# Performance work log

Measured on AMD Instinct MI355X. Metric: run time of the kernel, lower is better.

## Reference

```python
import jax, jax.numpy as jnp
import numpy as np

H = 8       # heads
D = 512     # hidden_size
DH = D // H # head dim
FF = 2048   # hardcoded FFN hidden in source


def _layernorm(x, g, b, eps=1e-5):
    mu = jnp.mean(x, axis=-1, keepdims=True)
    var = jnp.var(x, axis=-1, keepdims=True)
    return (x - mu) * jax.lax.rsqrt(var + eps) * g + b


def setup_inputs() -> dict:
    key = jax.random.key(0)
    ks = jax.random.split(key, 12)
    B, S = 2, 4096
    s = lambda fan_in: 1.0 / np.sqrt(fan_in)
    return {
        "reaction": jax.random.normal(ks[0], (B, S, D), dtype=jnp.float32),
        "mask": jnp.ones((B, 1, 1, S), dtype=jnp.int32),
        # attention weights stored as [in, out] (torch Linear weight.T)
        "Wq": jax.random.uniform(ks[1], (D, D), jnp.float32, -s(D), s(D)),
        "Wk": jax.random.uniform(ks[2], (D, D), jnp.float32, -s(D), s(D)),
        "Wv": jax.random.uniform(ks[3], (D, D), jnp.float32, -s(D), s(D)),
        "Wo": jax.random.uniform(ks[4], (D, D), jnp.float32, -s(D), s(D)),
        "bo": jnp.zeros((D,), jnp.float32),
        "W1": jax.random.uniform(ks[5], (D, FF), jnp.float32, -s(D), s(D)),
        "b1": jnp.zeros((FF,), jnp.float32),
        "W2": jax.random.uniform(ks[6], (FF, D), jnp.float32, -s(FF), s(FF)),
        "b2": jnp.zeros((D,), jnp.float32),
        "g_sa": jnp.ones((D,), jnp.float32),
        "b_sa": jnp.zeros((D,), jnp.float32),
        "g_ff": jnp.ones((D,), jnp.float32),
        "b_ff": jnp.zeros((D,), jnp.float32),
    }


def reference(reaction, mask, Wq, Wk, Wv, Wo, bo, W1, b1, W2, b2, g_sa, b_sa, g_ff, b_ff):
    B, S, _ = reaction.shape
    # --- self-attention part (pre-norm) ---
    x = _layernorm(reaction, g_sa, b_sa)
    q = (x @ Wq).reshape(B, S, H, DH)
    k = (x @ Wk).reshape(B, S, H, DH)
    v = (x @ Wv).reshape(B, S, H, DH)
    scale = DH ** (-0.5)
    scores = jnp.einsum('bqhd,bkhd->bhqk', q * scale, k)  # [B,H,S,S]
    scores = jnp.where(mask == 0, -jnp.inf, scores)
    att = jax.nn.softmax(scores, axis=-1)
    ctx = jnp.einsum('bhqk,bkhd->bqhd', att, v).reshape(B, S, D)
    attn_out = jax.nn.gelu(ctx @ Wo + bo, approximate=False)  # GELU after output proj (as in source)
    x = attn_out + reaction
    # --- feed-forward part (pre-norm) ---
    y = _layernorm(x, g_ff, b_ff)
    y = jax.nn.gelu(y @ W1 + b1, approximate=False) @ W2 + b2
    return y + x
```

## Files before the change

### kernel.cpp

```cpp
#include <hip/hip_runtime.h>
#include <hip/hip_bf16.h>
#include <math.h>

#define HN 8
#define DM 512
#define DHD 64
#define FFD 2048
#define BB 2
#define SS 4096
#define MT (BB*SS)

typedef __bf16 bf16_t;
typedef __bf16 bf16x8 __attribute__((ext_vector_type(8)));
typedef __bf16 bf16x4 __attribute__((ext_vector_type(4)));
typedef float  floatx4 __attribute__((ext_vector_type(4)));

__device__ __forceinline__ void async_copy16(const bf16_t* g, bf16_t* l) {
  __builtin_amdgcn_global_load_lds((const __attribute__((address_space(1))) void*)g,
                                   (__attribute__((address_space(3))) void*)l,
                                   16, 0, 0);
}

#if __has_builtin(__builtin_amdgcn_exp2f)
__device__ __forceinline__ float fast_exp2(float x) { return __builtin_amdgcn_exp2f(x); }
#else
__device__ __forceinline__ float fast_exp2(float x) { return __expf(x * 0.69314718056f); }
#endif

__device__ __forceinline__ float gelu_f(float x) {
  float y = 0.7978845608f * (x + 0.044715f * x * x * x);
  float e = fast_exp2(y * 2.885390082f);
  float th = 1.0f - 2.0f / (e + 1.0f);
  return 0.5f * x * (1.0f + th);
}

__global__ __launch_bounds__(256)
void ln_kernel(const float* __restrict__ x, const float* __restrict__ g,
               const float* __restrict__ be, bf16_t* __restrict__ out)
{
  const int wave = threadIdx.x >> 6, lane = threadIdx.x & 63;
  const int row = blockIdx.x * 4 + wave;
  const float* xr = x + (size_t)row * DM + lane * 8;
  float4 a = *(const float4*)xr;
  float4 c = *(const float4*)(xr + 4);
  float s  = (a.x + a.y) + (a.z + a.w) + (c.x + c.y) + (c.z + c.w);
  float s2 = (a.x*a.x + a.y*a.y) + (a.z*a.z + a.w*a.w)
           + (c.x*c.x + c.y*c.y) + (c.z*c.z + c.w*c.w);
#pragma unroll
  for (int o = 1; o < 64; o <<= 1) { s += __shfl_xor(s, o); s2 += __shfl_xor(s2, o); }
  const float mu = s * (1.0f / DM);
  const float rv = rsqrtf(s2 * (1.0f / DM) - mu * mu + 1e-5f);
  float4 g0 = *(const float4*)(g + lane * 8);
  float4 g1 = *(const float4*)(g + lane * 8 + 4);
  float4 b0 = *(const float4*)(be + lane * 8);
  float4 b1 = *(const float4*)(be + lane * 8 + 4);
  bf16x8 o8;
  o8[0] = (bf16_t)((a.x - mu) * rv * g0.x + b0.x);
  o8[1] = (bf16_t)((a.y - mu) * rv * g0.y + b0.y);
  o8[2] = (bf16_t)((a.z - mu) * rv * g0.z + b0.z);
  o8[3] = (bf16_t)((a.w - mu) * rv * g0.w + b0.w);
  o8[4] = (bf16_t)((c.x - mu) * rv * g1.x + b1.x);
  o8[5] = (bf16_t)((c.y - mu) * rv * g1.y + b1.y);
  o8[6] = (bf16_t)((c.z - mu) * rv * g1.z + b1.z);
  o8[7] = (bf16_t)((c.w - mu) * rv * g1.w + b1.w);
  *(bf16x8*)(out + (size_t)row * DM + lane * 8) = o8;
}

__global__ __launch_bounds__(256)
void prep_weights(const float* __restrict__ Wq, const float* __restrict__ Wk,
                  const float* __restrict__ Wv, const float* __restrict__ Wo,
                  const float* __restrict__ W1, const float* __restrict__ W2,
                  bf16_t* __restrict__ WqkvT, bf16_t* __restrict__ WoT,
                  bf16_t* __restrict__ W1T, bf16_t* __restrict__ W2T)
{
  const int bid = blockIdx.x;
  const float* src; bf16_t* dst; int Kd, Nd, n0, k0;
  if (bid < 768) {
    int seg = bid >> 8, t = bid & 255;
    src = (seg == 0) ? Wq : (seg == 1) ? Wk : Wv;
    dst = WqkvT + (size_t)seg * 512 * 512;
    Kd = 512; Nd = 512; n0 = (t & 15) * 32; k0 = (t >> 4) * 32;
  } else if (bid < 1024) {
    int t = bid - 768; src = Wo; dst = WoT;
    Kd = 512; Nd = 512; n0 = (t & 15) * 32; k0 = (t >> 4) * 32;
  } else if (bid < 2048) {
    int t = bid - 1024; src = W1; dst = W1T;
    Kd = 512; Nd = 2048; n0 = (t & 63) * 32; k0 = (t >> 6) * 32;
  } else {
    int t = bid - 2048; src = W2; dst = W2T;
    Kd = 2048; Nd = 512; n0 = (t & 15) * 32; k0 = (t >> 4) * 32;
  }
  __shared__ float tile[32][33];
  const int tx = threadIdx.x & 31, ty = threadIdx.x >> 5;
#pragma unroll
  for (int i = 0; i < 32; i += 8)
    tile[ty + i][tx] = src[(size_t)(k0 + ty + i) * Nd + n0 + tx];
  __syncthreads();
#pragma unroll
  for (int i = 0; i < 32; i += 8)
    dst[(size_t)(n0 + ty + i) * Kd + k0 + tx] = (bf16_t)tile[tx][ty + i];
}

template <int MI, int NJ, int EPI>
__global__ __launch_bounds__(256)
void gemm_bt(const bf16_t* __restrict__ A, const bf16_t* __restrict__ Bt,
             const int M, const int N, const int K,
             const float* __restrict__ bias, const float* __restrict__ res,
             bf16_t* __restrict__ outb, float* __restrict__ outf,
             bf16_t* __restrict__ out2, bf16_t* __restrict__ out3, const int ldt)
{
  constexpr int MTILE = 32 * MI, NTILE = 32 * NJ;
  constexpr int ACOPY = MTILE / 32;
  constexpr int BCOPY = NTILE / 32;
  __shared__ __align__(16) bf16_t lA[MTILE * 64];
  __shared__ __align__(16) bf16_t lB[NTILE * 64];
  const int tid = threadIdx.x;
  const int wave = tid >> 6, lane = tid & 63;
  const int wm = wave & 1, wn = wave >> 1;
  const int quad = lane >> 4, l16 = lane & 15;

  int srA[ACOPY > BCOPY ? ACOPY : BCOPY], scA[ACOPY > BCOPY ? ACOPY : BCOPY];
#pragma unroll
  for (int i = 0; i < (ACOPY > BCOPY ? ACOPY : BCOPY); ++i) {
    int flat = tid + 256 * i;
    int r = flat >> 3, ch = flat & 7;
    srA[i] = r;
    scA[i] = (ch ^ (r & 7)) * 8;
  }
  const bf16_t* Ab = A + (size_t)(blockIdx.x * MTILE) * K;
  const bf16_t* Bb = Bt + (size_t)(blockIdx.y * NTILE) * K;

  const floatx4 vzero = {0.f, 0.f, 0.f, 0.f};
  floatx4 acc[MI][NJ];
#pragma unroll
  for (int i = 0; i < MI; ++i)
#pragma unroll
    for (int j = 0; j < NJ; ++j) acc[i][j] = vzero;

  for (int k0 = 0; k0 < K; k0 += 64) {
    __syncthreads();
#pragma unroll
    for (int i = 0; i < ACOPY; ++i)
      async_copy16(Ab + (size_t)srA[i] * K + k0 + scA[i], lA + (tid + 256 * i) * 8);
#pragma unroll
    for (int i = 0; i < BCOPY; ++i)
      async_copy16(Bb + (size_t)srA[i] * K + k0 + scA[i], lB + (tid + 256 * i) * 8);
    __syncthreads();
#pragma unroll
    for (int c = 0; c < 2; ++c) {
      bf16x8 af[MI], bfv[NJ];
#pragma unroll
      for (int i = 0; i < MI; ++i)
        af[i] = *(const bf16x8*)(lA + (wm * 16 * MI + i * 16 + l16) * 64
                                 + (((c * 4 + quad) ^ (l16 & 7)) * 8));
#pragma unroll
      for (int j = 0; j < NJ; ++j)
        bfv[j] = *(const bf16x8*)(lB + (wn * 16 * NJ + j * 16 + l16) * 64
                                  + (((c * 4 + quad) ^ (l16 & 7)) * 8));
#pragma unroll
      for (int i = 0; i < MI; ++i)
#pragma unroll
        for (int j = 0; j < NJ; ++j)
          acc[i][j] = __builtin_amdgcn_mfma_f32_16x16x32_bf16(af[i], bfv[j], acc[i][j], 0, 0, 0);
    }
  }

  const int m00 = blockIdx.x * MTILE + wm * 16 * MI;
  const int n00 = blockIdx.y * NTILE + wn * 16 * NJ;
#pragma unroll
  for (int i = 0; i < MI; ++i) {
#pragma unroll
    for (int j = 0; j < NJ; ++j) {
      const int m0 = m00 + i * 16 + quad * 4;
      const int n  = n00 + j * 16 + l16;
      floatx4 v = acc[i][j];
      if (EPI == 2) {
        const float bb = bias[n];
#pragma unroll
        for (int r = 0; r < 4; ++r)
          outf[(size_t)(m0 + r) * N + n] = gelu_f(v[r] + bb) + res[(size_t)(m0 + r) * N + n];
      } else if (EPI == 3) {
        const float bb = bias[n];
#pragma unroll
        for (int r = 0; r < 4; ++r)
          outb[(size_t)(m0 + r) * N + n] = (bf16_t)gelu_f(v[r] + bb);
      } else if (EPI == 4) {
        const float bb = bias[n];
#pragma unroll
        for (int r = 0; r < 4; ++r)
          outf[(size_t)(m0 + r) * N + n] = v[r] + bb + res[(size_t)(m0 + r) * N + n];
      } else {
        const int seg = blockIdx.y >> 2;
        if (seg == 0) {
#pragma unroll
          for (int r = 0; r < 4; ++r)
            outb[(size_t)(m0 + r) * 512 + n] = (bf16_t)(v[r] * 0.180336879f);
        } else if (seg == 1) {
#pragma unroll
          for (int r = 0; r < 4; ++r) out2[(size_t)(m0 + r) * 512 + (n - 512)] = (bf16_t)v[r];
        } else {
          const int o = m0 & 31;
          const int p0 = (m0 & ~31) + ((o >> 2) & 3) * 8 + ((o >> 4) << 2);
          bf16x4 pk = {(bf16_t)v[0], (bf16_t)v[1], (bf16_t)v[2], (bf16_t)v[3]};
          *(bf16x4*)(out3 + (size_t)(n - 1024) * ldt + p0) = pk;
        }
      }
    }
  }
}

__global__ __launch_bounds__(256, 2)
void attn_kernel(const bf16_t* __restrict__ qm, const bf16_t* __restrict__ km,
                 const bf16_t* __restrict__ vtm, const int* __restrict__ mask,
                 bf16_t* __restrict__ ctx)
{
  const int flat = blockIdx.x + 32 * (blockIdx.y + 8 * blockIdx.z);
  const int swz = (flat & 7) * 64 + (flat >> 3);
  const int b = swz >> 8, h = (swz >> 5) & 7;
  const int q0 = (swz & 31) * 128;
  const int tid = threadIdx.x;
  const int wave = tid >> 6, lane = tid & 63;
  const int quad = lane >> 4, l16 = lane & 15;

  __shared__ __align__(16) bf16_t lK[2][128 * DHD];
  __shared__ __align__(16) bf16_t lV[2][DHD * 128];
  __shared__ int sclean[4];

  const int* maskb = mask + b * SS;

  unsigned um = 0xFFFFFFFFu;
#pragma unroll
  for (int i = 0; i < 4; ++i) {
    int4 m = *(const int4*)(maskb + tid * 16 + i * 4);
    um = min(um, min(min((unsigned)m.x, (unsigned)m.y), min((unsigned)m.z, (unsigned)m.w)));
  }
#pragma unroll
  for (int o = 1; o < 64; o <<= 1) um = min(um, (unsigned)__shfl_xor((int)um, o));
  if (lane == 0) sclean[wave] = (int)um;
  __syncthreads();
  const bool clean = (min(min((unsigned)sclean[0], (unsigned)sclean[1]),
                          min((unsigned)sclean[2], (unsigned)sclean[3])) != 0u);

  const size_t qrow0 = (size_t)b * SS + q0;
  bf16x8 qa[2][2];
#pragma unroll
  for (int mb = 0; mb < 2; ++mb)
#pragma unroll
    for (int cc = 0; cc < 2; ++cc)
      qa[mb][cc] = *(const bf16x8*)(qm + (qrow0 + wave * 32 + mb * 16 + l16) * DM
                                    + h * DHD + cc * 32 + quad * 8);

  const floatx4 vzero = {0.f, 0.f, 0.f, 0.f};
  floatx4 cacc[2][4];
  float lsum[2] = {0.f, 0.f};
#pragma unroll
  for (int mb = 0; mb < 2; ++mb)
#pragma unroll
    for (int nb = 0; nb < 4; ++nb) cacc[mb][nb] = vzero;

  const bf16_t* Kb = km + (size_t)b * SS * DM + h * DHD;
  const bf16_t* Vb = vtm + (size_t)(h * DHD) * MT + (size_t)b * SS;

  const bf16_t* pk[4]; const bf16_t* pv[4];
#pragma unroll
  for (int i = 0; i < 4; ++i) {
    int p = tid + 256 * i;
    int key = p >> 3, cs = (p & 7) ^ (key & 7);
    pk[i] = Kb + (size_t)key * DM + cs * 8;
    int dh = p >> 4, cs2 = (p & 15) ^ (dh & 7);
    pv[i] = Vb + (size_t)dh * MT + cs2 * 8;
  }

  auto stage = [&](int buf, int s0) {
#pragma unroll
    for (int i = 0; i < 4; ++i) {
      int p8 = (tid + 256 * i) * 8;
      async_copy16(pk[i] + (size_t)s0 * DM, lK[buf] + p8);
      async_copy16(pv[i] + s0, lV[buf] + p8);
    }
  };

  auto compute = [&](const bf16_t* __restrict__ lKb, const bf16_t* __restrict__ lVb,
                     int s0) {
#pragma unroll
    for (int c = 0; c < 4; ++c) {
      floatx4 sa[2], sb[2];
      sa[0] = vzero; sa[1] = vzero; sb[0] = vzero; sb[1] = vzero;
#pragma unroll
      for (int cc = 0; cc < 2; ++cc) {
        const int ko = ((cc * 4 + quad) ^ (l16 & 7)) * 8;
        bf16x8 kf0 = *(const bf16x8*)(lKb + (c * 32 + l16) * 64 + ko);
        bf16x8 kf1 = *(const bf16x8*)(lKb + (c * 32 + 16 + l16) * 64 + ko);
        __builtin_amdgcn_s_setprio(1);
#pragma unroll
        for (int mb = 0; mb < 2; ++mb) {
          sa[mb] = __builtin_amdgcn_mfma_f32_16x16x32_bf16(kf0, qa[mb][cc], sa[mb], 0, 0, 0);
          sb[mb] = __builtin_amdgcn_mfma_f32_16x16x32_bf16(kf1, qa[mb][cc], sb[mb], 0, 0, 0);
        }
        __builtin_amdgcn_s_setprio(0);
      }

      if (!clean) {
        const int4 m0 = *(const int4*)(maskb + s0 + c * 32 + quad * 4);
        const int4 m1 = *(const int4*)(maskb + s0 + c * 32 + 16 + quad * 4);
#pragma unroll
        for (int mb = 0; mb < 2; ++mb) {
          if (m0.x == 0) sa[mb][0] = -1e30f;
          if (m0.y == 0) sa[mb][1] = -1e30f;
          if (m0.z == 0) sa[mb][2] = -1e30f;
          if (m0.w == 0) sa[mb][3] = -1e30f;
          if (m1.x == 0) sb[mb][0] = -1e30f;
          if (m1.y == 0) sb[mb][1] = -1e30f;
          if (m1.z == 0) sb[mb][2] = -1e30f;
          if (m1.w == 0) sb[mb][3] = -1e30f;
        }
      }

      bf16x8 pf[2];
#pragma unroll
      for (int mb = 0; mb < 2; ++mb) {
        float e0 = fast_exp2(sa[mb][0]), e1 = fast_exp2(sa[mb][1]);
        float e2 = fast_exp2(sa[mb][2]), e3 = fast_exp2(sa[mb][3]);
        float e4 = fast_exp2(sb[mb][0]), e5 = fast_exp2(sb[mb][1]);
        float e6 = fast_exp2(sb[mb][2]), e7 = fast_exp2(sb[mb][3]);
        lsum[mb] += ((e0 + e1) + (e2 + e3)) + ((e4 + e5) + (e6 + e7));
        pf[mb][0] = (bf16_t)e0; pf[mb][1] = (bf16_t)e1;
        pf[mb][2] = (bf16_t)e2; pf[mb][3] = (bf16_t)e3;
        pf[mb][4] = (bf16_t)e4; pf[mb][5] = (bf16_t)e5;
        pf[mb][6] = (bf16_t)e6; pf[mb][7] = (bf16_t)e7;
      }
      const int ch = (c * 4 + quad) ^ (l16 & 7);
      __builtin_amdgcn_s_setprio(1);
#pragma unroll
      for (int nb = 0; nb < 4; ++nb) {
        bf16x8 av = *(const bf16x8*)(lVb + (nb * 16 + l16) * 128 + ch * 8);
        cacc[0][nb] = __builtin_amdgcn_mfma_f32_16x16x32_bf16(av, pf[0], cacc[0][nb], 0, 0, 0);
        cacc[1][nb] = __builtin_amdgcn_mfma_f32_16x16x32_bf16(av, pf[1], cacc[1][nb], 0, 0, 0);
      }
      __builtin_amdgcn_s_setprio(0);
    }
  };

  stage(0, 0);
#pragma unroll 1
  for (int s0 = 0; s0 < SS; s0 += 256) {
    __syncthreads();
    stage(1, s0 + 128);
    compute(lK[0], lV[0], s0);
    __syncthreads();
    if (s0 + 256 < SS) stage(0, s0 + 256);
    compute(lK[1], lV[1], s0 + 128);
  }

#pragma unroll
  for (int mb = 0; mb < 2; ++mb) {
    float tot = lsum[mb];
    tot += __shfl_xor(tot, 16);
    tot += __shfl_xor(tot, 32);
    const float inv = 1.0f / tot;
    const size_t qrow = qrow0 + wave * 32 + mb * 16 + l16;
#pragma unroll
    for (int nb = 0; nb < 4; ++nb) {
      bf16x4 o = {(bf16_t)(cacc[mb][nb][0] * inv), (bf16_t)(cacc[mb][nb][1] * inv),
                  (bf16_t)(cacc[mb][nb][2] * inv), (bf16_t)(cacc[mb][nb][3] * inv)};
      *(bf16x4*)(ctx + qrow * DM + h * DHD + nb * 16 + quad * 4) = o;
    }
  }
}

extern "C" void kernel_launch(void* const* d_in, const int* in_sizes, int n_in,
                              void* d_out, int out_size, void* d_ws, size_t ws_size,
                              hipStream_t stream)
{
  (void)in_sizes; (void)n_in; (void)out_size; (void)ws_size;
  const float* reaction = (const float*)d_in[0];
  const int*   mask     = (const int*)d_in[1];
  const float* Wq = (const float*)d_in[2];
  const float* Wk = (const float*)d_in[3];
  const float* Wv = (const float*)d_in[4];
  const float* Wo = (const float*)d_in[5];
  const float* bo = (const float*)d_in[6];
  const float* W1 = (const float*)d_in[7];
  const float* b1 = (const float*)d_in[8];
  const float* W2 = (const float*)d_in[9];
  const float* b2 = (const float*)d_in[10];
  const float* g_sa = (const float*)d_in[11];
  const float* b_sa = (const float*)d_in[12];
  const float* g_ff = (const float*)d_in[13];
  const float* b_ff = (const float*)d_in[14];
  float* out = (float*)d_out;

  char* ws = (char*)d_ws;
  size_t off = 0;
  auto take = [&](size_t bytes) -> char* {
    char* p = ws + off;
    off += (bytes + 255) & ~(size_t)255;
    return p;
  };

  bf16_t* xln   = (bf16_t*)take((size_t)MT * DM * 2);
  bf16_t* WqkvT = (bf16_t*)take((size_t)3 * DM * DM * 2);
  bf16_t* WoT   = (bf16_t*)take((size_t)DM * DM * 2);
  bf16_t* W1T   = (bf16_t*)take((size_t)FFD * DM * 2);
  bf16_t* W2T   = (bf16_t*)take((size_t)DM * FFD * 2);
  bf16_t* qb    = (bf16_t*)take((size_t)MT * DM * 2);
  bf16_t* kb    = (bf16_t*)take((size_t)MT * DM * 2);
  bf16_t* vtb   = (bf16_t*)take((size_t)DM * MT * 2);
  bf16_t* ctx   = (bf16_t*)take((size_t)MT * DM * 2);
  float*  x2    = (float*)take((size_t)MT * DM * 4);
  bf16_t* yb    = xln;
  bf16_t* hb    = qb;

  ln_kernel<<<MT / 4, 256, 0, stream>>>(reaction, g_sa, b_sa, xln);
  prep_weights<<<3072, 256, 0, stream>>>(Wq, Wk, Wv, Wo, W1, W2, WqkvT, WoT, W1T, W2T);

  gemm_bt<4, 4, 5><<<dim3(64, 12), 256, 0, stream>>>(xln, WqkvT, MT, 3 * DM, DM,
                                                     nullptr, nullptr, qb, nullptr, kb, vtb, MT);

  attn_kernel<<<dim3(SS / 128, HN, BB), 256, 0, stream>>>(qb, kb, vtb, mask, ctx);

  gemm_bt<4, 2, 2><<<dim3(64, 8), 256, 0, stream>>>(ctx, WoT, MT, DM, DM,
                                                    bo, reaction, nullptr, x2, nullptr, nullptr, 0);

  ln_kernel<<<MT / 4, 256, 0, stream>>>(x2, g_ff, b_ff, yb);
  gemm_bt<4, 4, 3><<<dim3(64, 16), 256, 0, stream>>>(yb, W1T, MT, FFD, DM,
                                                     b1, nullptr, hb, nullptr, nullptr, nullptr, 0);
  gemm_bt<4, 2, 4><<<dim3(64, 8), 256, 0, stream>>>(hb, W2T, MT, DM, FFD,
                                                    b2, x2, nullptr, out, nullptr, nullptr, 0);
}
```

Measured before the change: 271.1 us.

## Fuse LN with weight prep and software-pipeline LDS fragment loads in attention

Merges the first layernorm and the weight transpose/convert kernels into one launch, with the block index choosing which job a block does, which removes one kernel launch and its tail. In the attention kernel the mask-free path gets its own compute loop that double-buffers K and V fragment reads from LDS in registers, so the next chunk's loads are issued while the current chunk's MFMAs run. The masked path is kept separate. The pipelining raises register pressure, which could lower occupancy or cause spills.

```diff
diff --git a/kernel.cpp b/kernel.cpp
--- a/kernel.cpp
+++ b/kernel.cpp
@@ -32,6 +32,72 @@
   float e = fast_exp2(y * 2.885390082f);
   float th = 1.0f - 2.0f / (e + 1.0f);
   return 0.5f * x * (1.0f + th);
+}
+
+__global__ __launch_bounds__(256)
+void prep_ln(const float* __restrict__ x, const float* __restrict__ g,
+             const float* __restrict__ be, bf16_t* __restrict__ out,
+             const float* __restrict__ Wq, const float* __restrict__ Wk,
+             const float* __restrict__ Wv, const float* __restrict__ Wo,
+             const float* __restrict__ W1, const float* __restrict__ W2,
+             bf16_t* __restrict__ WqkvT, bf16_t* __restrict__ WoT,
+             bf16_t* __restrict__ W1T, bf16_t* __restrict__ W2T)
+{
+  __shared__ float tile[32][33];
+  if (blockIdx.x < 2048) {
+    const int wave = threadIdx.x >> 6, lane = threadIdx.x & 63;
+    const int row = blockIdx.x * 4 + wave;
+    const float* xr = x + (size_t)row * DM + lane * 8;
+    float4 a = *(const float4*)xr;
+    float4 c = *(const float4*)(xr + 4);
+    float s  = (a.x + a.y) + (a.z + a.w) + (c.x + c.y) + (c.z + c.w);
+    float s2 = (a.x*a.x + a.y*a.y) + (a.z*a.z + a.w*a.w)
+             + (c.x*c.x + c.y*c.y) + (c.z*c.z + c.w*c.w);
+#pragma unroll
+    for (int o = 1; o < 64; o <<= 1) { s += __shfl_xor(s, o); s2 += __shfl_xor(s2, o); }
+    const float mu = s * (1.0f / DM);
+    const float rv = rsqrtf(s2 * (1.0f / DM) - mu * mu + 1e-5f);
+    float4 g0 = *(const float4*)(g + lane * 8);
+    float4 g1 = *(const float4*)(g + lane * 8 + 4);
+    float4 b0 = *(const float4*)(be + lane * 8);
+    float4 b1 = *(const float4*)(be + lane * 8 + 4);
+    bf16x8 o8;
+    o8[0] = (bf16_t)((a.x - mu) * rv * g0.x + b0.x);
+    o8[1] = (bf16_t)((a.y - mu) * rv * g0.y + b0.y);
+    o8[2] = (bf16_t)((a.z - mu) * rv * g0.z + b0.z);
+    o8[3] = (bf16_t)((a.w - mu) * rv * g0.w + b0.w);
+    o8[4] = (bf16_t)((c.x - mu) * rv * g1.x + b1.x);
+    o8[5] = (bf16_t)((c.y - mu) * rv * g1.y + b1.y);
+    o8[6] = (bf16_t)((c.z - mu) * rv * g1.z + b1.z);
+    o8[7] = (bf16_t)((c.w - mu) * rv * g1.w + b1.w);
+    *(bf16x8*)(out + (size_t)row * DM + lane * 8) = o8;
+    return;
+  }
+  const int bid = blockIdx.x - 2048;
+  const float* src; bf16_t* dst; int Kd, Nd, n0, k0;
+  if (bid < 768) {
+    int seg = bid >> 8, t = bid & 255;
+    src = (seg == 0) ? Wq : (seg == 1) ? Wk : Wv;
+    dst = WqkvT + (size_t)seg * 512 * 512;
+    Kd = 512; Nd = 512; n0 = (t & 15) * 32; k0 = (t >> 4) * 32;
+  } else if (bid < 1024) {
+    int t = bid - 768; src = Wo; dst = WoT;
+    Kd = 512; Nd = 512; n0 = (t & 15) * 32; k0 = (t >> 4) * 32;
+  } else if (bid < 2048) {
+    int t = bid - 1024; src = W1; dst = W1T;
+    Kd = 512; Nd = 2048; n0 = (t & 63) * 32; k0 = (t >> 6) * 32;
+  } else {
+    int t = bid - 2048; src = W2; dst = W2T;
+    Kd = 2048; Nd = 512; n0 = (t & 15) * 32; k0 = (t >> 4) * 32;
+  }
+  const int tx = threadIdx.x & 31, ty = threadIdx.x >> 5;
+#pragma unroll
+  for (int i = 0; i < 32; i += 8)
+    tile[ty + i][tx] = src[(size_t)(k0 + ty + i) * Nd + n0 + tx];
+  __syncthreads();
+#pragma unroll
+  for (int i = 0; i < 32; i += 8)
+    dst[(size_t)(n0 + ty + i) * Kd + k0 + tx] = (bf16_t)tile[tx][ty + i];
 }
 
 __global__ __launch_bounds__(256)
@@ -66,41 +132,6 @@
   *(bf16x8*)(out + (size_t)row * DM + lane * 8) = o8;
 }
 
-__global__ __launch_bounds__(256)
-void prep_weights(const float* __restrict__ Wq, const float* __restrict__ Wk,
-                  const float* __restrict__ Wv, const float* __restrict__ Wo,
-                  const float* __restrict__ W1, const float* __restrict__ W2,
-                  bf16_t* __restrict__ WqkvT, bf16_t* __restrict__ WoT,
-                  bf16_t* __restrict__ W1T, bf16_t* __restrict__ W2T)
-{
-  const int bid = blockIdx.x;
-  const float* src; bf16_t* dst; int Kd, Nd, n0, k0;
-  if (bid < 768) {
-    int seg = bid >> 8, t = bid & 255;
-    src = (seg == 0) ? Wq : (seg == 1) ? Wk : Wv;
-    dst = WqkvT + (size_t)seg * 512 * 512;
-    Kd = 512; Nd = 512; n0 = (t & 15) * 32; k0 = (t >> 4) * 32;
-  } else if (bid < 1024) {
-    int t = bid - 768; src = Wo; dst = WoT;
-    Kd = 512; Nd = 512; n0 = (t & 15) * 32; k0 = (t >> 4) * 32;
-  } else if (bid < 2048) {
-    int t = bid - 1024; src = W1; dst = W1T;
-    Kd = 512; Nd = 2048; n0 = (t & 63) * 32; k0 = (t >> 6) * 32;
-  } else {
-    int t = bid - 2048; src = W2; dst = W2T;
-    Kd = 2048; Nd = 512; n0 = (t & 15) * 32; k0 = (t >> 4) * 32;
-  }
-  __shared__ float tile[32][33];
-  const int tx = threadIdx.x & 31, ty = threadIdx.x >> 5;
-#pragma unroll
-  for (int i = 0; i < 32; i += 8)
-    tile[ty + i][tx] = src[(size_t)(k0 + ty + i) * Nd + n0 + tx];
-  __syncthreads();
-#pragma unroll
-  for (int i = 0; i < 32; i += 8)
-    dst[(size_t)(n0 + ty + i) * Kd + k0 + tx] = (bf16_t)tile[tx][ty + i];
-}
-
 template <int MI, int NJ, int EPI>
 __global__ __launch_bounds__(256)
 void gemm_bt(const bf16_t* __restrict__ A, const bf16_t* __restrict__ Bt,
@@ -280,27 +311,104 @@
     }
   };
 
-  auto compute = [&](const bf16_t* __restrict__ lKb, const bf16_t* __restrict__ lVb,
-                     int s0) {
-#pragma unroll
-    for (int c = 0; c < 4; ++c) {
-      floatx4 sa[2], sb[2];
-      sa[0] = vzero; sa[1] = vzero; sb[0] = vzero; sb[1] = vzero;
+  auto exp_pv = [&](floatx4 sa[2], floatx4 sb[2], const bf16x8 av[4]) {
+    bf16x8 pf[2];
+#pragma unroll
+    for (int mb = 0; mb < 2; ++mb) {
+      float e0 = fast_exp2(sa[mb][0]), e1 = fast_exp2(sa[mb][1]);
+      float e2 = fast_exp2(sa[mb][2]), e3 = fast_exp2(sa[mb][3]);
+      float e4 = fast_exp2(sb[mb][0]), e5 = fast_exp2(sb[mb][1]);
+      float e6 = fast_exp2(sb[mb][2]), e7 = fast_exp2(sb[mb][3]);
+      lsum[mb] += ((e0 + e1) + (e2 + e3)) + ((e4 + e5) + (e6 + e7));
+      pf[mb][0] = (bf16_t)e0; pf[mb][1] = (bf16_t)e1;
+      pf[mb][2] = (bf16_t)e2; pf[mb][3] = (bf16_t)e3;
+      pf[mb][4] = (bf16_t)e4; pf[mb][5] = (bf16_t)e5;
+      pf[mb][6] = (bf16_t)e6; pf[mb][7] = (bf16_t)e7;
+    }
+    __builtin_amdgcn_s_setprio(1);
+#pragma unroll
+    for (int nb = 0; nb < 4; ++nb) {
+      cacc[0][nb] = __builtin_amdgcn_mfma_f32_16x16x32_bf16(av[nb], pf[0], cacc[0][nb], 0, 0, 0);
+      cacc[1][nb] = __builtin_amdgcn_mfma_f32_16x16x32_bf16(av[nb], pf[1], cacc[1][nb], 0, 0, 0);
+    }
+    __builtin_amdgcn_s_setprio(0);
+  };
+
+  if (clean) {
+    auto compute_clean = [&](const bf16_t* __restrict__ lKb,
+                             const bf16_t* __restrict__ lVb) {
+      bf16x8 kf[2][2][2];
+      bf16x8 av[2][4];
 #pragma unroll
       for (int cc = 0; cc < 2; ++cc) {
         const int ko = ((cc * 4 + quad) ^ (l16 & 7)) * 8;
-        bf16x8 kf0 = *(const bf16x8*)(lKb + (c * 32 + l16) * 64 + ko);
-        bf16x8 kf1 = *(const bf16x8*)(lKb + (c * 32 + 16 + l16) * 64 + ko);
+        kf[0][cc][0] = *(const bf16x8*)(lKb + (l16) * 64 + ko);
+        kf[0][cc][1] = *(const bf16x8*)(lKb + (16 + l16) * 64 + ko);
+      }
+#pragma unroll
+      for (int nb = 0; nb < 4; ++nb)
+        av[0][nb] = *(const bf16x8*)(lVb + (nb * 16 + l16) * 128
+                                     + ((quad ^ (l16 & 7)) * 8));
+#pragma unroll
+      for (int c = 0; c < 4; ++c) {
+        const int buf = c & 1, nbuf = buf ^ 1;
+        floatx4 sa[2], sb[2];
+        sa[0] = vzero; sa[1] = vzero; sb[0] = vzero; sb[1] = vzero;
         __builtin_amdgcn_s_setprio(1);
 #pragma unroll
-        for (int mb = 0; mb < 2; ++mb) {
-          sa[mb] = __builtin_amdgcn_mfma_f32_16x16x32_bf16(kf0, qa[mb][cc], sa[mb], 0, 0, 0);
-          sb[mb] = __builtin_amdgcn_mfma_f32_16x16x32_bf16(kf1, qa[mb][cc], sb[mb], 0, 0, 0);
+        for (int cc = 0; cc < 2; ++cc)
+#pragma unroll
+          for (int mb = 0; mb < 2; ++mb) {
+            sa[mb] = __builtin_amdgcn_mfma_f32_16x16x32_bf16(kf[buf][cc][0], qa[mb][cc], sa[mb], 0, 0, 0);
+            sb[mb] = __builtin_amdgcn_mfma_f32_16x16x32_bf16(kf[buf][cc][1], qa[mb][cc], sb[mb], 0, 0, 0);
+          }
+        __builtin_amdgcn_s_setprio(0);
+        if (c < 3) {
+#pragma unroll
+          for (int cc = 0; cc < 2; ++cc) {
+            const int ko = (((cc * 4 + quad)) ^ (l16 & 7)) * 8;
+            kf[nbuf][cc][0] = *(const bf16x8*)(lKb + ((c + 1) * 32 + l16) * 64 + ko);
+            kf[nbuf][cc][1] = *(const bf16x8*)(lKb + ((c + 1) * 32 + 16 + l16) * 64 + ko);
+          }
+          const int chn = ((c + 1) * 4 + quad) ^ (l16 & 7);
+#pragma unroll
+          for (int nb = 0; nb < 4; ++nb)
+            av[nbuf][nb] = *(const bf16x8*)(lVb + (nb * 16 + l16) * 128 + chn * 8);
         }
-        __builtin_amdgcn_s_setprio(0);
+        exp_pv(sa, sb, av[buf]);
       }
-
-      if (!clean) {
+    };
+
+    stage(0, 0);
+#pragma unroll 1
+    for (int s0 = 0; s0 < SS; s0 += 256) {
+      __syncthreads();
+      stage(1, s0 + 128);
+      compute_clean(lK[0], lV[0]);
+      __syncthreads();
+      if (s0 + 256 < SS) stage(0, s0 + 256);
+      compute_clean(lK[1], lV[1]);
+    }
+  } else {
+    auto compute_masked = [&](const bf16_t* __restrict__ lKb,
+                              const bf16_t* __restrict__ lVb, int s0) {
+#pragma unroll
+      for (int c = 0; c < 4; ++c) {
+        floatx4 sa[2], sb[2];
+        sa[0] = vzero; sa[1] = vzero; sb[0] = vzero; sb[1] = vzero;
+#pragma unroll
+        for (int cc = 0; cc < 2; ++cc) {
+          const int ko = ((cc * 4 + quad) ^ (l16 & 7)) * 8;
+          bf16x8 kf0 = *(const bf16x8*)(lKb + (c * 32 + l16) * 64 + ko);
+          bf16x8 kf1 = *(const bf16x8*)(lKb + (c * 32 + 16 + l16) * 64 + ko);
+          __builtin_amdgcn_s_setprio(1);
+#pragma unroll
+          for (int mb = 0; mb < 2; ++mb) {
+            sa[mb] = __builtin_amdgcn_mfma_f32_16x16x32_bf16(kf0, qa[mb][cc], sa[mb], 0, 0, 0);
+            sb[mb] = __builtin_amdgcn_mfma_f32_16x16x32_bf16(kf1, qa[mb][cc], sb[mb], 0, 0, 0);
+          }
+          __builtin_amdgcn_s_setprio(0);
+        }
         const int4 m0 = *(const int4*)(maskb + s0 + c * 32 + quad * 4);
         const int4 m1 = *(const int4*)(maskb + s0 + c * 32 + 16 + quad * 4);
 #pragma unroll
@@ -314,42 +422,25 @@
           if (m1.z == 0) sb[mb][2] = -1e30f;
           if (m1.w == 0) sb[mb][3] = -1e30f;
         }
+        const int ch = (c * 4 + quad) ^ (l16 & 7);
+        bf16x8 av[4];
+#pragma unroll
+        for (int nb = 0; nb < 4; ++nb)
+          av[nb] = *(const bf16x8*)(lVb + (nb * 16 + l16) * 128 + ch * 8);
+        exp_pv(sa, sb, av);
       }
-
-      bf16x8 pf[2];
-#pragma unroll
-      for (int mb = 0; mb < 2; ++mb) {
-        float e0 = fast_exp2(sa[mb][0]), e1 = fast_exp2(sa[mb][1]);
-        float e2 = fast_exp2(sa[mb][2]), e3 = fast_exp2(sa[mb][3]);
-        float e4 = fast_exp2(sb[mb][0]), e5 = fast_exp2(sb[mb][1]);
-        float e6 = fast_exp2(sb[mb][2]), e7 = fast_exp2(sb[mb][3]);
-        lsum[mb] += ((e0 + e1) + (e2 + e3)) + ((e4 + e5) + (e6 + e7));
-        pf[mb][0] = (bf16_t)e0; pf[mb][1] = (bf16_t)e1;
-        pf[mb][2] = (bf16_t)e2; pf[mb][3] = (bf16_t)e3;
-        pf[mb][4] = (bf16_t)e4; pf[mb][5] = (bf16_t)e5;
-        pf[mb][6] = (bf16_t)e6; pf[mb][7] = (bf16_t)e7;
-      }
-      const int ch = (c * 4 + quad) ^ (l16 & 7);
-      __builtin_amdgcn_s_setprio(1);
-#pragma unroll
-      for (int nb = 0; nb < 4; ++nb) {
-        bf16x8 av = *(const bf16x8*)(lVb + (nb * 16 + l16) * 128 + ch * 8);
-        cacc[0][nb] = __builtin_amdgcn_mfma_f32_16x16x32_bf16(av, pf[0], cacc[0][nb], 0, 0, 0);
-        cacc[1][nb] = __builtin_amdgcn_mfma_f32_16x16x32_bf16(av, pf[1], cacc[1][nb], 0, 0, 0);
-      }
-      __builtin_amdgcn_s_setprio(0);
-    }
-  };
-
-  stage(0, 0);
+    };
+
+    stage(0, 0);
 #pragma unroll 1
-  for (int s0 = 0; s0 < SS; s0 += 256) {
-    __syncthreads();
-    stage(1, s0 + 128);
-    compute(lK[0], lV[0], s0);
-    __syncthreads();
-    if (s0 + 256 < SS) stage(0, s0 + 256);
-    compute(lK[1], lV[1], s0 + 128);
+    for (int s0 = 0; s0 < SS; s0 += 256) {
+      __syncthreads();
+      stage(1, s0 + 128);
+      compute_masked(lK[0], lV[0], s0);
+      __syncthreads();
+      if (s0 + 256 < SS) stage(0, s0 + 256);
+      compute_masked(lK[1], lV[1], s0 + 128);
+    }
   }
 
 #pragma unroll
@@ -411,8 +502,8 @@
   bf16_t* yb    = xln;
   bf16_t* hb    = qb;
 
-  ln_kernel<<<MT / 4, 256, 0, stream>>>(reaction, g_sa, b_sa, xln);
-  prep_weights<<<3072, 256, 0, stream>>>(Wq, Wk, Wv, Wo, W1, W2, WqkvT, WoT, W1T, W2T);
+  prep_ln<<<5120, 256, 0, stream>>>(reaction, g_sa, b_sa, xln,
+                                    Wq, Wk, Wv, Wo, W1, W2, WqkvT, WoT, W1T, W2T);
 
   gemm_bt<4, 4, 5><<<dim3(64, 12), 256, 0, stream>>>(xln, WqkvT, MT, 3 * DM, DM,
                                                      nullptr, nullptr, qb, nullptr, kb, vtb, MT);
```

Result: no change. 274.7 us (+1.3%).
